# Kernel tuning notes

Hardware: AMD Instinct MI355X
Metric: run time of the kernel (lower is better)

Reference implementation:

```python
import jax, jax.numpy as jnp
import numpy as np

IN_FEATURES = 4096
OUT_FEATURES = 4096
INPUT_SCALE = 0.05
OUTPUT_SCALE = 0.05


def setup_inputs() -> dict:
    key = jax.random.key(0)
    k_x, k_w, k_ws = jax.random.split(key, 3)
    # int8 activations (already quantized upstream in W8A8 pipeline)
    x = jax.random.randint(k_x, (4, 2048, IN_FEATURES), -128, 128, dtype=jnp.int32).astype(jnp.int8)
    # simulate per-tensor absmax quantization of an fp32 weight
    w_fp = jax.random.normal(k_w, (OUT_FEATURES, IN_FEATURES), dtype=jnp.float32) * 0.02
    weight_scale = jnp.max(jnp.abs(w_fp)) / 127.0
    w_int8 = jnp.clip(jnp.round(w_fp / weight_scale), -128, 127).astype(jnp.int8)
    weight = w_int8.T  # stored as [in_features, out_features], matching int8_weight.t()
    a = jnp.array([[INPUT_SCALE / OUTPUT_SCALE]], dtype=jnp.float32)
    b = jnp.reshape(weight_scale.astype(jnp.float32), (1, 1))
    return {"x": x, "weight": weight, "a": a, "b": b}


def reference(x, weight, a, b):
    # round and saturate back to int8 (output dtype == x.dtype == int8).
    x_shape = x.shape
    x2 = x.reshape(-1, x_shape[-1]).astype(jnp.int32)          # [N, D]
    acc = jnp.matmul(x2, weight.astype(jnp.int32))             # [N, O] int32 accum
    scale = (a * b)[0, 0]                                      # alpha = in_scale*w_scale/out_scale
    y = jnp.clip(jnp.round(acc.astype(jnp.float32) * scale), -128.0, 127.0).astype(jnp.int8)
    return y.reshape(*x_shape[:-1], -1)
```

## Files before the change

### kernel.cpp

```cpp
#include <hip/hip_runtime.h>
#include <stdint.h>

typedef __attribute__((ext_vector_type(4))) int int4v;
typedef __attribute__((ext_vector_type(16))) int int16v;
typedef __attribute__((ext_vector_type(4))) uint32_t uint4v;

#define M_DIM 8192
#define N_DIM 4096
#define K_DIM 4096


__global__ void pack_a_perm(const int* __restrict__ x, uint4v* __restrict__ a8) {
    const int g = blockIdx.x * blockDim.x + threadIdx.x;
    const int w0 = (g & 3) * 4;
    const int chunk = g >> 2;
    const int* base = x + (size_t)chunk * 64;
    int4v L[4];
#pragma unroll
    for (int j = 0; j < 4; ++j) L[j] = *(const int4v*)(base + j * 16 + w0);
    uint4v outv;
#pragma unroll
    for (int wi = 0; wi < 4; ++wi) {
        outv[wi] = (uint32_t)(L[0][wi] & 0xff) | ((uint32_t)(L[1][wi] & 0xff) << 8) |
                   ((uint32_t)(L[2][wi] & 0xff) << 16) | ((uint32_t)(L[3][wi] & 0xff) << 24);
    }
    a8[g] = outv;
}

__global__ void transpose_b_perm(const int* __restrict__ w, int8_t* __restrict__ bt) {
    const int t = threadIdx.x;
    const int kt = blockIdx.y * 64;
    const int n0 = blockIdx.x * 64;
    const int c4 = t & 3;
    const int n = t >> 2;
    const int w0 = c4 * 4;
    const int* col = w + (size_t)kt * N_DIM + n0 + n;
    uint4v outv;
#pragma unroll
    for (int wi = 0; wi < 4; ++wi) {
        uint32_t p = 0;
#pragma unroll
        for (int j = 0; j < 4; ++j) {
            uint32_t b = (uint32_t)(col[(size_t)(w0 + wi + 16 * j) * N_DIM] & 0xff);
            p |= b << (8 * j);
        }
        outv[wi] = p;
    }
    *(uint4v*)&bt[(size_t)(n0 + n) * K_DIM + kt + w0 * 4] = outv;
}

__device__ inline void async16(const void* g, void* l) {
    __builtin_amdgcn_global_load_lds(
        (const __attribute__((address_space(1))) uint32_t*)g,
        (__attribute__((address_space(3))) uint32_t*)l, 16, 0, 0);
}

#define SB() __builtin_amdgcn_sched_barrier(0)
#define BAR() do { SB(); __builtin_amdgcn_s_barrier(); SB(); } while (0)

__global__ void __launch_bounds__(512, 2)
gemm_kernel(const int8_t* __restrict__ A, const int8_t* __restrict__ Bt,
            const float* __restrict__ pa, const float* __restrict__ pb,
            int* __restrict__ out) {
    __shared__ int8_t smem[131072];

    const int t = threadIdx.x;
    const int lane = t & 63;
    const int wave = t >> 6;

    int wg = (int)blockIdx.x;
    wg = (wg & 7) * 64 + (wg >> 3);
    const int bx = wg & 15;
    const int by = wg >> 4;
    const int m0 = by * 256;
    const int n0 = bx * 256;

    const int wm = (wave >> 2) * 128;
    const int wn = (wave & 3) * 64;
    const float scale = pa[0] * pb[0];

    const int srow = 32 * wave + (lane & 15);
    const int ssl = (lane >> 4) * 16;
    const int8_t* pA0 = A + (size_t)(m0 + srow) * K_DIM + ssl;
    const int8_t* pA1 = pA0 + (size_t)16 * K_DIM;
    const int8_t* pB0 = Bt + (size_t)(n0 + srow) * K_DIM + ssl;
    const int8_t* pB1 = pB0 + (size_t)16 * K_DIM;
    const int ldsA0 = wave * 2048;
    const int ldsA1 = ldsA0 + 1024;
    const int ldsB0 = 16384 + ldsA0;
    const int ldsB1 = ldsB0 + 1024;

    const int rl = lane & 31;
    const int hl = lane >> 5;
    const int raB = ((wm + rl) >> 4) * 1024 + (rl & 15) * 16 + hl * 256;
    const int rbB = 16384 + ((wn + rl) >> 4) * 1024 + (rl & 15) * 16 + hl * 256;

    int16v acc[4][2];
#pragma unroll
    for (int mi = 0; mi < 4; ++mi)
#pragma unroll
        for (int j = 0; j < 2; ++j)
#pragma unroll
            for (int r = 0; r < 16; ++r) acc[mi][j][r] = 0;

    int4v afE[4], bfE[2], afO[4], bfO[2];

#define STAGE(TT) do {                                                   \
        const int b_ = ((TT) & 3) * 32768;                               \
        const int kt_ = ((TT) & 63) * 64;        \
        async16(pA0 + kt_, smem + b_ + ldsA0);                           \
        async16(pA1 + kt_, smem + b_ + ldsA1);                           \
        async16(pB0 + kt_, smem + b_ + ldsB0);                           \
        async16(pB1 + kt_, smem + b_ + ldsB1);                           \
    } while (0)

#define RD_SET(AF, BF, BUF, KO) do {                                     \
        const int ab_ = (BUF) * 32768 + (KO);                            \
        AF[0] = *(const int4v*)&smem[ab_ + raB + 0 * 2048];              \
        AF[1] = *(const int4v*)&smem[ab_ + raB + 1 * 2048];              \
        AF[2] = *(const int4v*)&smem[ab_ + raB + 2 * 2048];              \
        AF[3] = *(const int4v*)&smem[ab_ + raB + 3 * 2048];              \
        BF[0] = *(const int4v*)&smem[ab_ + rbB + 0 * 2048];              \
        BF[1] = *(const int4v*)&smem[ab_ + rbB + 1 * 2048];              \
    } while (0)

#define MM(AF, BF) do {                                                  \
        __builtin_amdgcn_s_setprio(1);                                   \
        _Pragma("unroll")                                                \
        for (int mi = 0; mi < 4; ++mi)                                   \
            _Pragma("unroll")                                            \
            for (int j = 0; j < 2; ++j)                                  \
                acc[mi][j] = __builtin_amdgcn_mfma_i32_32x32x32_i8(      \
                    AF[mi], BF[j], acc[mi][j], 0, 0, 0);                 \
        __builtin_amdgcn_s_setprio(0);                                   \
    } while (0)

    STAGE(0); STAGE(1); STAGE(2);
    asm volatile("s_waitcnt vmcnt(8)" ::: "memory");
    BAR();
    RD_SET(afE, bfE, 0, 0);

#pragma unroll 1
    for (int tt = 0; tt < 64; ++tt) {
        STAGE(tt + 3);
        RD_SET(afO, bfO, tt & 3, 512);
        SB();
        MM(afE, bfE);
        SB();
        asm volatile("s_waitcnt vmcnt(8)" ::: "memory");
        BAR();
        RD_SET(afE, bfE, (tt + 1) & 3, 0);
        SB();
        MM(afO, bfO);
        BAR();
    }

    asm volatile("s_waitcnt vmcnt(0) lgkmcnt(0)" ::: "memory");

    const int col = lane & 31;
    const int rbase = (lane >> 5) * 4;
#pragma unroll
    for (int mi = 0; mi < 4; ++mi)
#pragma unroll
        for (int j = 0; j < 2; ++j)
#pragma unroll
            for (int r = 0; r < 16; ++r) {
                const int rowf = rbase + (r & 3) + 8 * (r >> 2);
                float v = (float)acc[mi][j][r] * scale;
                v = rintf(v);
                v = fminf(127.f, fmaxf(-128.f, v));
                out[(size_t)(m0 + wm + mi * 32 + rowf) * N_DIM +
                    (n0 + wn + j * 32 + col)] = (int)v;
            }
#undef STAGE
#undef RD_SET
#undef MM
}

extern "C" void kernel_launch(void* const* d_in, const int* in_sizes, int n_in,
                              void* d_out, int out_size, void* d_ws, size_t ws_size,
                              hipStream_t stream) {
    const int* x = (const int*)d_in[0];
    const int* w = (const int*)d_in[1];
    const float* pa = (const float*)d_in[2];
    const float* pb = (const float*)d_in[3];
    int* out = (int*)d_out;

    int8_t* a8 = (int8_t*)d_ws;
    int8_t* bt8 = a8 + (size_t)M_DIM * K_DIM;

    const int nwords_a = M_DIM * K_DIM / 16;
    pack_a_perm<<<nwords_a / 256, 256, 0, stream>>>(x, (uint4v*)a8);
    transpose_b_perm<<<dim3(N_DIM / 64, K_DIM / 64), 256, 0, stream>>>(w, bt8);
    gemm_kernel<<<dim3(512), dim3(512), 0, stream>>>(a8, bt8, pa, pb, out);
}
```

Baseline: 418.1 us.

## Restructure GEMM main loop to double-buffered 128-wide K tiles with split-phase loads

Replaces the 4-stage ring of 64-wide K tiles with 2 buffers of 128-wide K tiles. Each tile is loaded in halves, with the B and A loads interleaved between MFMA groups. Fragment reads are split by M-half with partial lgkmcnt waits, so LDS reads overlap the first MFMA batch. The aim is fewer barriers per K step and better overlap of global-to-LDS copies with compute, at the cost of shallower prefetch depth and more hand-tuned wait counts that must stay correct.

Measured after the change: 418.1 us. Within noise of the previous version (+0.0%).

```diff
diff --git a/kernel.cpp b/kernel.cpp
--- a/kernel.cpp
+++ b/kernel.cpp
@@ -80,20 +80,16 @@
     const float scale = pa[0] * pb[0];
 
     const int srow = 32 * wave + (lane & 15);
-    const int ssl = (lane >> 4) * 16;
-    const int8_t* pA0 = A + (size_t)(m0 + srow) * K_DIM + ssl;
-    const int8_t* pA1 = pA0 + (size_t)16 * K_DIM;
-    const int8_t* pB0 = Bt + (size_t)(n0 + srow) * K_DIM + ssl;
-    const int8_t* pB1 = pB0 + (size_t)16 * K_DIM;
-    const int ldsA0 = wave * 2048;
-    const int ldsA1 = ldsA0 + 1024;
-    const int ldsB0 = 16384 + ldsA0;
-    const int ldsB1 = ldsB0 + 1024;
+    const int shalf = (lane >> 4) * 16;
+    const int8_t* pA = A + (size_t)(m0 + srow) * K_DIM + shalf;
+    const int8_t* pB = Bt + (size_t)(n0 + srow) * K_DIM + shalf;
+    const int ldsA = wave * 4096;
+    const int ldsB = 32768 + wave * 4096;
 
     const int rl = lane & 31;
-    const int hl = lane >> 5;
-    const int raB = ((wm + rl) >> 4) * 1024 + (rl & 15) * 16 + hl * 256;
-    const int rbB = 16384 + ((wn + rl) >> 4) * 1024 + (rl & 15) * 16 + hl * 256;
+    const int hlp = (lane >> 5) * 256;
+    const int raB = ((wm + rl) >> 4) * 2048 + (rl & 15) * 16 + hlp;
+    const int rbB = 32768 + ((wn + rl) >> 4) * 2048 + (rl & 15) * 16 + hlp;
 
     int16v acc[4][2];
 #pragma unroll
@@ -103,55 +99,82 @@
 #pragma unroll
             for (int r = 0; r < 16; ++r) acc[mi][j][r] = 0;
 
-    int4v afE[4], bfE[2], afO[4], bfO[2];
-
-#define STAGE(TT) do {                                                   \
-        const int b_ = ((TT) & 3) * 32768;                               \
-        const int kt_ = ((TT) & 63) * 64;        \
-        async16(pA0 + kt_, smem + b_ + ldsA0);                           \
-        async16(pA1 + kt_, smem + b_ + ldsA1);                           \
-        async16(pB0 + kt_, smem + b_ + ldsB0);                           \
-        async16(pB1 + kt_, smem + b_ + ldsB1);                           \
-    } while (0)
-
-#define RD_SET(AF, BF, BUF, KO) do {                                     \
-        const int ab_ = (BUF) * 32768 + (KO);                            \
-        AF[0] = *(const int4v*)&smem[ab_ + raB + 0 * 2048];              \
-        AF[1] = *(const int4v*)&smem[ab_ + raB + 1 * 2048];              \
-        AF[2] = *(const int4v*)&smem[ab_ + raB + 2 * 2048];              \
-        AF[3] = *(const int4v*)&smem[ab_ + raB + 3 * 2048];              \
-        BF[0] = *(const int4v*)&smem[ab_ + rbB + 0 * 2048];              \
-        BF[1] = *(const int4v*)&smem[ab_ + rbB + 1 * 2048];              \
-    } while (0)
-
-#define MM(AF, BF) do {                                                  \
-        __builtin_amdgcn_s_setprio(1);                                   \
-        _Pragma("unroll")                                                \
-        for (int mi = 0; mi < 4; ++mi)                                   \
-            _Pragma("unroll")                                            \
-            for (int j = 0; j < 2; ++j)                                  \
-                acc[mi][j] = __builtin_amdgcn_mfma_i32_32x32x32_i8(      \
-                    AF[mi], BF[j], acc[mi][j], 0, 0, 0);                 \
-        __builtin_amdgcn_s_setprio(0);                                   \
-    } while (0)
-
-    STAGE(0); STAGE(1); STAGE(2);
-    asm volatile("s_waitcnt vmcnt(8)" ::: "memory");
+    int4v afX[2][2], afY[2][2], bfX[2][2];
+
+#define ST2(P, LDSOFF, TT, H) do {                                        \
+        const int b_ = ((TT) & 1) * 65536;                                \
+        const int kt_ = ((TT) & 31) * 128 + (H) * 64;     \
+        async16((P) + kt_, smem + b_ + (LDSOFF) + (H) * 1024);            \
+        async16((P) + kt_ + (size_t)16 * K_DIM,                           \
+                smem + b_ + (LDSOFF) + (H) * 1024 + 2048);                \
+    } while (0)
+
+#define RD_A(AF, BUF, KH, MH) do {                                        \
+        const int a_ = (BUF) * 65536 + raB + (MH) * 8192 + (KH) * 1024;   \
+        AF[0][0] = *(const int4v*)&smem[a_ + 0 * 4096 + 0 * 512];         \
+        AF[0][1] = *(const int4v*)&smem[a_ + 0 * 4096 + 1 * 512];         \
+        AF[1][0] = *(const int4v*)&smem[a_ + 1 * 4096 + 0 * 512];         \
+        AF[1][1] = *(const int4v*)&smem[a_ + 1 * 4096 + 1 * 512];         \
+    } while (0)
+
+#define RD_B(BF, BUF, KH) do {                                            \
+        const int a_ = (BUF) * 65536 + rbB + (KH) * 1024;                 \
+        BF[0][0] = *(const int4v*)&smem[a_ + 0 * 4096 + 0 * 512];         \
+        BF[0][1] = *(const int4v*)&smem[a_ + 0 * 4096 + 1 * 512];         \
+        BF[1][0] = *(const int4v*)&smem[a_ + 1 * 4096 + 0 * 512];         \
+        BF[1][1] = *(const int4v*)&smem[a_ + 1 * 4096 + 1 * 512];         \
+    } while (0)
+
+#define MM8(AF, BF, MH) do {                                              \
+        __builtin_amdgcn_s_setprio(1);                                    \
+        _Pragma("unroll")                                                 \
+        for (int kw = 0; kw < 2; ++kw)                                    \
+            _Pragma("unroll")                                             \
+            for (int i = 0; i < 2; ++i)                                   \
+                _Pragma("unroll")                                         \
+                for (int j = 0; j < 2; ++j)                               \
+                    acc[(MH) * 2 + i][j] = __builtin_amdgcn_mfma_i32_32x32x32_i8( \
+                        AF[i][kw], BF[j][kw], acc[(MH) * 2 + i][j], 0, 0, 0); \
+        __builtin_amdgcn_s_setprio(0);                                    \
+    } while (0)
+
+    ST2(pB, ldsB, 0, 0); ST2(pA, ldsA, 0, 0);
+    ST2(pB, ldsB, 0, 1); ST2(pA, ldsA, 0, 1);
+    asm volatile("s_waitcnt vmcnt(4)" ::: "memory");
     BAR();
-    RD_SET(afE, bfE, 0, 0);
 
 #pragma unroll 1
-    for (int tt = 0; tt < 64; ++tt) {
-        STAGE(tt + 3);
-        RD_SET(afO, bfO, tt & 3, 512);
-        SB();
-        MM(afE, bfE);
-        SB();
-        asm volatile("s_waitcnt vmcnt(8)" ::: "memory");
-        BAR();
-        RD_SET(afE, bfE, (tt + 1) & 3, 0);
-        SB();
-        MM(afO, bfO);
+    for (int tt = 0; tt < 32; ++tt) {
+        const int c = tt & 1;
+        ST2(pB, ldsB, tt + 1, 0);
+        RD_A(afX, c, 0, 0); RD_B(bfX, c, 0);
+        RD_A(afY, c, 0, 1);
+        SB();
+        asm volatile("s_waitcnt lgkmcnt(4)" ::: "memory");
+        SB();
+        MM8(afX, bfX, 0);
+        BAR();
+        ST2(pA, ldsA, tt + 1, 0);
+        SB();
+        asm volatile("s_waitcnt lgkmcnt(0)" ::: "memory");
+        SB();
+        MM8(afY, bfX, 1);
+        asm volatile("s_waitcnt vmcnt(4)" ::: "memory");
+        BAR();
+        ST2(pB, ldsB, tt + 1, 1);
+        RD_A(afX, c, 1, 0); RD_B(bfX, c, 1);
+        RD_A(afY, c, 1, 1);
+        SB();
+        asm volatile("s_waitcnt lgkmcnt(4)" ::: "memory");
+        SB();
+        MM8(afX, bfX, 0);
+        BAR();
+        ST2(pA, ldsA, tt + 1, 1);
+        SB();
+        asm volatile("s_waitcnt lgkmcnt(0)" ::: "memory");
+        SB();
+        MM8(afY, bfX, 1);
+        asm volatile("s_waitcnt vmcnt(4)" ::: "memory");
         BAR();
     }
 
@@ -172,9 +195,10 @@
                 out[(size_t)(m0 + wm + mi * 32 + rowf) * N_DIM +
                     (n0 + wn + j * 32 + col)] = (int)v;
             }
-#undef STAGE
-#undef RD_SET
-#undef MM
+#undef ST2
+#undef RD_A
+#undef RD_B
+#undef MM8
 }
 
 extern "C" void kernel_launch(void* const* d_in, const int* in_sizes, int n_in,
```
